# Kernel tuning notes

Hardware: AMD Instinct MI355X
Metric: run time of the kernel (lower is better)

## Reference

```python
import jax, jax.numpy as jnp
import numpy as np

B, IN, OUT = 128, 1024, 1024
BETA, THRESHOLD, RESET = 0.99, 1.0, 0.8
TAU_POS, TAU_NEG = 20.0, 20.0
A_POS, A_NEG = 0.005, 0.005


def setup_inputs() -> dict:
    key = jax.random.key(0)
    k1, k2, k3, k4, k5 = jax.random.split(key, 5)
    in_spikes = (jax.random.uniform(k1, (B, IN)) < 0.1).astype(jnp.float32)
    # nn.Linear default init: U(-1/sqrt(in), 1/sqrt(in))
    bound = 1.0 / np.sqrt(IN)
    W = jax.random.uniform(k2, (OUT, IN), minval=-bound, maxval=bound, dtype=jnp.float32)
    membrane = jax.random.normal(k3, (B, OUT), dtype=jnp.float32) * 0.5
    # trace timers (time since last spike), random in [0, 50)
    delta_pre = jax.random.uniform(k4, (B, IN), dtype=jnp.float32) * 50.0
    delta_fire = jax.random.uniform(k5, (B, OUT), dtype=jnp.float32) * 50.0
    return {"in_spikes": in_spikes, "W": W, "membrane": membrane,
            "delta_pre": delta_pre, "delta_fire": delta_fire}


def reference(in_spikes, W, membrane, delta_pre, delta_fire):
    # dense projection (bias is unused in the original forward)
    weighted = jnp.matmul(in_spikes, W.T)                      # (B, OUT)
    # LIF neuron
    mem = membrane * BETA + weighted
    spike = (mem > THRESHOLD).astype(jnp.float32)
    mem = jnp.where(spike > 0, mem - RESET, mem)
    # trace updates: increment, reset-to-zero where a spike occurred
    dp = jnp.where(in_spikes > 0, 0.0, delta_pre + 1.0)        # (B, IN)
    df = jnp.where(spike > 0, 0.0, delta_fire + 1.0)           # (B, OUT)
    # pairwise timing difference: (B, IN, OUT)
    delta_t = df[:, None, :] - dp[:, :, None]
    potentiation = (delta_t > 0) * (A_POS * jnp.exp(-delta_t / TAU_POS))
    depression = (delta_t < 0) * (A_NEG * jnp.exp(delta_t / TAU_NEG))
    weight_changes = potentiation - depression                 # (B, IN, OUT)
    avg_weight_changes = weight_changes.mean(axis=0).T         # (OUT, IN)
    new_W = W + avg_weight_changes
    return spike, new_W, mem
```

## Files before the change

### kernel.cpp

```cpp
#include <hip/hip_runtime.h>
#include <cmath>

#define Bb   128
#define INN  1024
#define OUTN 1024
#define BBCH 32
#define A_TOT   (0.005f / 128.0f)
#define INV_TAU (1.0f / 20.0f)

__global__ __launch_bounds__(256) void transpose_k(const float* __restrict__ W,
                                                   float* __restrict__ Wt) {
    __shared__ float tile[32][33];
    const int bx = blockIdx.x;
    const int by = blockIdx.y;
    const int x = threadIdx.x & 31;
    const int y = threadIdx.x >> 5;
#pragma unroll
    for (int j = 0; j < 4; j++) {
        int o = by * 32 + y + j * 8;
        tile[y + j * 8][x] = W[(size_t)o * INN + bx * 32 + x];
    }
    __syncthreads();
#pragma unroll
    for (int j = 0; j < 4; j++) {
        int i = bx * 32 + y + j * 8;
        Wt[(size_t)i * OUTN + by * 32 + x] = tile[x][y + j * 8];
    }
}

__global__ __launch_bounds__(256) void spmv_lif_pack_k(
    const float* __restrict__ in_spikes, const float* __restrict__ Wt,
    const float* __restrict__ membrane, const float* __restrict__ delta_pre,
    const float* __restrict__ delta_fire,
    float2* __restrict__ OPack, float2* __restrict__ IPack,
    float* __restrict__ out_spike, float* __restrict__ out_mem) {
    __shared__ int sIdx[INN];
    __shared__ int sCount;
    const int b = blockIdx.x;
    const int z = blockIdx.y;
    const int t = threadIdx.x;

    if (t < 64) {
        int base = 0;
#pragma unroll
        for (int c = 0; c < 16; c++) {
            float s = in_spikes[(size_t)b * INN + c * 64 + t];
            unsigned long long m = __ballot(s > 0.0f);
            if (s > 0.0f) {
                int pos = base + __popcll(m & ((1ULL << t) - 1ULL));
                sIdx[pos] = c * 64 + t;
            }
            base += __popcll(m);
        }
        if (t == 0) sCount = base;
    }
    __syncthreads();

    const int n = sCount;
    const int o = z * 256 + t;
    float acc = 0.0f;
    int j = 0;
    for (; j + 8 <= n; j += 8) {
        float w0 = Wt[(size_t)sIdx[j + 0] * OUTN + o];
        float w1 = Wt[(size_t)sIdx[j + 1] * OUTN + o];
        float w2 = Wt[(size_t)sIdx[j + 2] * OUTN + o];
        float w3 = Wt[(size_t)sIdx[j + 3] * OUTN + o];
        float w4 = Wt[(size_t)sIdx[j + 4] * OUTN + o];
        float w5 = Wt[(size_t)sIdx[j + 5] * OUTN + o];
        float w6 = Wt[(size_t)sIdx[j + 6] * OUTN + o];
        float w7 = Wt[(size_t)sIdx[j + 7] * OUTN + o];
        acc += ((w0 + w1) + (w2 + w3)) + ((w4 + w5) + (w6 + w7));
    }
    for (; j < n; j++) acc += Wt[(size_t)sIdx[j] * OUTN + o];

    const int n_bo = b * OUTN + o;
    float mem = membrane[n_bo] * 0.99f + acc;
    float s = (mem > 1.0f) ? 1.0f : 0.0f;
    mem = (s > 0.0f) ? mem - 0.8f : mem;
    out_spike[n_bo] = s;
    out_mem[n_bo] = mem;

    float df = (s > 0.0f) ? 0.0f : delta_fire[n_bo] + 1.0f;
    OPack[n_bo] = make_float2(expf(-df * INV_TAU), -A_TOT * expf(df * INV_TAU));

    const int n_bi = b * INN + o;
    float sp = in_spikes[n_bi];
    float dp = (sp > 0.0f) ? 0.0f : delta_pre[n_bi] + 1.0f;
    IPack[n_bi] = make_float2(A_TOT * expf(dp * INV_TAU), expf(-dp * INV_TAU));
}

__global__ __launch_bounds__(256, 4) void stdp_k(const float* __restrict__ W,
                                                 const float2* __restrict__ OPack,
                                                 const float2* __restrict__ IPack,
                                                 float* __restrict__ outW) {
    __shared__ float2 sO[BBCH][32];
    __shared__ float2 sI[BBCH][32];
    const int t  = threadIdx.x;
    const int o0 = blockIdx.x * 32;
    const int i0 = blockIdx.y * 32;
    const int tx = t & 15;
    const int ty = t >> 4;

    float acc[2][2] = {{0.f, 0.f}, {0.f, 0.f}};

    for (int cb = 0; cb < Bb / BBCH; cb++) {
#pragma unroll
        for (int r = 0; r < 4; r++) {
            int idx = r * 256 + t;
            int bb = idx >> 5, col = idx & 31;
            int bgl = cb * BBCH + bb;
            sO[bb][col] = OPack[(size_t)bgl * OUTN + o0 + col];
            sI[bb][col] = IPack[(size_t)bgl * INN  + i0 + col];
        }
        __syncthreads();
#pragma unroll
        for (int bb = 0; bb < BBCH; bb++) {
            float4 op = *(const float4*)&sO[bb][2 * ty];
            float4 ip = *(const float4*)&sI[bb][2 * tx];
            bool c00 = op.x < ip.y;
            acc[0][0] = fmaf(c00 ? op.x : op.y, c00 ? ip.x : ip.y, acc[0][0]);
            bool c01 = op.x < ip.w;
            acc[0][1] = fmaf(c01 ? op.x : op.y, c01 ? ip.z : ip.w, acc[0][1]);
            bool c10 = op.z < ip.y;
            acc[1][0] = fmaf(c10 ? op.z : op.w, c10 ? ip.x : ip.y, acc[1][0]);
            bool c11 = op.z < ip.w;
            acc[1][1] = fmaf(c11 ? op.z : op.w, c11 ? ip.z : ip.w, acc[1][1]);
        }
        __syncthreads();
    }

#pragma unroll
    for (int a = 0; a < 2; a++) {
        const int o = o0 + 2 * ty + a;
        const size_t off = (size_t)o * INN + i0 + 2 * tx;
        float2 w = *(const float2*)&W[off];
        *(float2*)&outW[off] = make_float2(w.x + acc[a][0], w.y + acc[a][1]);
    }
}

extern "C" void kernel_launch(void* const* d_in, const int* in_sizes, int n_in,
                              void* d_out, int out_size, void* d_ws, size_t ws_size,
                              hipStream_t stream) {
    const float* in_spikes  = (const float*)d_in[0];
    const float* W          = (const float*)d_in[1];
    const float* membrane   = (const float*)d_in[2];
    const float* delta_pre  = (const float*)d_in[3];
    const float* delta_fire = (const float*)d_in[4];

    float* out_spike = (float*)d_out;
    float* out_W     = out_spike + (size_t)Bb * OUTN;
    float* out_mem   = out_W + (size_t)OUTN * INN;

    float* ws     = (float*)d_ws;
    float* Wt     = ws;
    float2* OPack = (float2*)(Wt + (size_t)INN * OUTN);
    float2* IPack = OPack + (size_t)Bb * OUTN;

    hipLaunchKernelGGL(transpose_k, dim3(INN / 32, OUTN / 32), dim3(256), 0, stream,
                       W, Wt);
    hipLaunchKernelGGL(spmv_lif_pack_k, dim3(Bb, 4), dim3(256), 0, stream,
                       in_spikes, Wt, membrane, delta_pre, delta_fire,
                       OPack, IPack, out_spike, out_mem);
    hipLaunchKernelGGL(stdp_k, dim3(OUTN / 32, INN / 32), dim3(256), 0, stream,
                       W, OPack, IPack, out_W);
}
```

Baseline: 107.0 us.

## Pack STDP factors as bf16 pairs and select via integer min/max

Result: faster. 101.5 us (-5.1%).

```diff
diff --git a/kernel.cpp b/kernel.cpp
--- a/kernel.cpp
+++ b/kernel.cpp
@@ -1,12 +1,17 @@
 #include <hip/hip_runtime.h>
+#include <cstdint>
 #include <cmath>
 
 #define Bb   128
 #define INN  1024
 #define OUTN 1024
-#define BBCH 32
 #define A_TOT   (0.005f / 128.0f)
 #define INV_TAU (1.0f / 20.0f)
+
+__device__ __forceinline__ uint32_t rne_bf16(float f) {
+    uint32_t u = __float_as_uint(f);
+    return (u + 0x7fffu + ((u >> 16) & 1u)) >> 16;
+}
 
 __global__ __launch_bounds__(256) void transpose_k(const float* __restrict__ W,
                                                    float* __restrict__ Wt) {
@@ -32,7 +37,7 @@
     const float* __restrict__ in_spikes, const float* __restrict__ Wt,
     const float* __restrict__ membrane, const float* __restrict__ delta_pre,
     const float* __restrict__ delta_fire,
-    float2* __restrict__ OPack, float2* __restrict__ IPack,
+    uint32_t* __restrict__ OPackB, uint32_t* __restrict__ IPackB,
     float* __restrict__ out_spike, float* __restrict__ out_mem) {
     __shared__ int sIdx[INN];
     __shared__ int sCount;
@@ -81,50 +86,57 @@
     out_mem[n_bo] = mem;
 
     float df = (s > 0.0f) ? 0.0f : delta_fire[n_bo] + 1.0f;
-    OPack[n_bo] = make_float2(expf(-df * INV_TAU), -A_TOT * expf(df * INV_TAU));
+    float Oy = expf(-df * INV_TAU);
+    float Oz = -A_TOT * expf(df * INV_TAU);
+    OPackB[n_bo] = (rne_bf16(Oy) << 16) | rne_bf16(Oz);
 
     const int n_bi = b * INN + o;
     float sp = in_spikes[n_bi];
     float dp = (sp > 0.0f) ? 0.0f : delta_pre[n_bi] + 1.0f;
-    IPack[n_bi] = make_float2(A_TOT * expf(dp * INV_TAU), expf(-dp * INV_TAU));
+    float Iz = expf(-dp * INV_TAU);
+    float Iy = A_TOT * expf(dp * INV_TAU);
+    IPackB[n_bi] = (rne_bf16(Iz) << 16) | rne_bf16(Iy);
 }
 
 __global__ __launch_bounds__(256, 4) void stdp_k(const float* __restrict__ W,
-                                                 const float2* __restrict__ OPack,
-                                                 const float2* __restrict__ IPack,
+                                                 const uint32_t* __restrict__ OPackB,
+                                                 const uint32_t* __restrict__ IPackB,
                                                  float* __restrict__ outW) {
-    __shared__ float2 sO[BBCH][32];
-    __shared__ float2 sI[BBCH][32];
+    __shared__ uint32_t sO[32][32];
+    __shared__ uint32_t sI[32][32];
     const int t  = threadIdx.x;
     const int o0 = blockIdx.x * 32;
     const int i0 = blockIdx.y * 32;
     const int tx = t & 15;
     const int ty = t >> 4;
+    const int srow = t >> 3;
+    const int scol = (t & 7) * 4;
 
     float acc[2][2] = {{0.f, 0.f}, {0.f, 0.f}};
 
-    for (int cb = 0; cb < Bb / BBCH; cb++) {
-#pragma unroll
-        for (int r = 0; r < 4; r++) {
-            int idx = r * 256 + t;
-            int bb = idx >> 5, col = idx & 31;
-            int bgl = cb * BBCH + bb;
-            sO[bb][col] = OPack[(size_t)bgl * OUTN + o0 + col];
-            sI[bb][col] = IPack[(size_t)bgl * INN  + i0 + col];
-        }
+    for (int cb = 0; cb < Bb / 32; cb++) {
+        const int bgl = cb * 32 + srow;
+        *(uint4*)&sO[srow][scol] =
+            *(const uint4*)&OPackB[(size_t)bgl * OUTN + o0 + scol];
+        *(uint4*)&sI[srow][scol] =
+            *(const uint4*)&IPackB[(size_t)bgl * INN + i0 + scol];
         __syncthreads();
 #pragma unroll
-        for (int bb = 0; bb < BBCH; bb++) {
-            float4 op = *(const float4*)&sO[bb][2 * ty];
-            float4 ip = *(const float4*)&sI[bb][2 * tx];
-            bool c00 = op.x < ip.y;
-            acc[0][0] = fmaf(c00 ? op.x : op.y, c00 ? ip.x : ip.y, acc[0][0]);
-            bool c01 = op.x < ip.w;
-            acc[0][1] = fmaf(c01 ? op.x : op.y, c01 ? ip.z : ip.w, acc[0][1]);
-            bool c10 = op.z < ip.y;
-            acc[1][0] = fmaf(c10 ? op.z : op.w, c10 ? ip.x : ip.y, acc[1][0]);
-            bool c11 = op.z < ip.w;
-            acc[1][1] = fmaf(c11 ? op.z : op.w, c11 ? ip.z : ip.w, acc[1][1]);
+        for (int bb = 0; bb < 32; bb++) {
+            uint2 po = *(const uint2*)&sO[bb][2 * ty];
+            uint2 pi = *(const uint2*)&sI[bb][2 * tx];
+#pragma unroll
+            for (int a = 0; a < 2; a++) {
+                uint32_t o_ = (a == 0) ? po.x : po.y;
+#pragma unroll
+                for (int c = 0; c < 2; c++) {
+                    uint32_t i_ = (c == 0) ? pi.x : pi.y;
+                    uint32_t key = min(o_, i_);
+                    uint32_t pay = max(o_, i_) << 16;
+                    acc[a][c] = fmaf(__uint_as_float(key),
+                                     __uint_as_float(pay), acc[a][c]);
+                }
+            }
         }
         __syncthreads();
     }
@@ -151,16 +163,16 @@
     float* out_W     = out_spike + (size_t)Bb * OUTN;
     float* out_mem   = out_W + (size_t)OUTN * INN;
 
-    float* ws     = (float*)d_ws;
-    float* Wt     = ws;
-    float2* OPack = (float2*)(Wt + (size_t)INN * OUTN);
-    float2* IPack = OPack + (size_t)Bb * OUTN;
+    float* ws        = (float*)d_ws;
+    float* Wt        = ws;
+    uint32_t* OPackB = (uint32_t*)(Wt + (size_t)INN * OUTN);
+    uint32_t* IPackB = OPackB + (size_t)Bb * OUTN;
 
     hipLaunchKernelGGL(transpose_k, dim3(INN / 32, OUTN / 32), dim3(256), 0, stream,
                        W, Wt);
     hipLaunchKernelGGL(spmv_lif_pack_k, dim3(Bb, 4), dim3(256), 0, stream,
                        in_spikes, Wt, membrane, delta_pre, delta_fire,
-                       OPack, IPack, out_spike, out_mem);
+                       OPackB, IPackB, out_spike, out_mem);
     hipLaunchKernelGGL(stdp_k, dim3(OUTN / 32, INN / 32), dim3(256), 0, stream,
-                       W, OPack, IPack, out_W);
+                       W, OPackB, IPackB, out_W);
 }
```
